# Kernel optimization log

Hardware: AMD Instinct MI355X
Metric: run time of the kernel (lower is better)

The kernel has to match this reference:

```python
import jax, jax.numpy as jnp
import numpy as np

NUM_HEADS = 32
NUM_KV_HEADS = 8
NUM_GROUPS = NUM_HEADS // NUM_KV_HEADS  # 4
HEAD_DIM = 64
HIDDEN = 2048
ROPE_THETA = 10000.0


def rotate_half(x):
    half = x.shape[-1] // 2
    x1, x2 = x[..., :half], x[..., half:]
    return jnp.concatenate([-x2, x1], axis=-1)


def rope_cos_sin(seq_len, dtype):
    inv_freq = 1.0 / (ROPE_THETA ** (jnp.arange(0, HEAD_DIM, 2, dtype=jnp.float32) / HEAD_DIM))
    pos = jnp.arange(seq_len, dtype=jnp.float32)
    freqs = jnp.outer(pos, inv_freq)          # [S, HEAD_DIM/2]
    emb = jnp.concatenate([freqs, freqs], axis=-1)  # [S, HEAD_DIM]
    return jnp.cos(emb).astype(dtype), jnp.sin(emb).astype(dtype)


def setup_inputs() -> dict:
    key = jax.random.key(0)
    k0, k1, k2, k3, k4 = jax.random.split(key, 5)
    B, S = 2, 2048
    scale = 0.02
    return {
        "hidden_states": jax.random.normal(k0, (B, S, HIDDEN), dtype=jnp.float32),
        "Wq": jax.random.normal(k1, (NUM_HEADS * HEAD_DIM, HIDDEN), dtype=jnp.float32) * scale,
        "Wk": jax.random.normal(k2, (NUM_KV_HEADS * HEAD_DIM, HIDDEN), dtype=jnp.float32) * scale,
        "Wv": jax.random.normal(k3, (NUM_KV_HEADS * HEAD_DIM, HIDDEN), dtype=jnp.float32) * scale,
        "Wo": jax.random.normal(k4, (HIDDEN, NUM_HEADS * HEAD_DIM), dtype=jnp.float32) * scale,
    }


def reference(hidden_states, Wq, Wk, Wv, Wo):
    B, S, _ = hidden_states.shape
    # projections (nn.Linear: x @ W.T)
    q = (hidden_states @ Wq.T).reshape(B, S, NUM_HEADS, HEAD_DIM).transpose(0, 2, 1, 3)
    k = (hidden_states @ Wk.T).reshape(B, S, NUM_KV_HEADS, HEAD_DIM).transpose(0, 2, 1, 3)
    v = (hidden_states @ Wv.T).reshape(B, S, NUM_KV_HEADS, HEAD_DIM).transpose(0, 2, 1, 3)

    cos, sin = rope_cos_sin(S, q.dtype)  # [S, HEAD_DIM]
    cos = cos[None, None]                # [1,1,S,HEAD_DIM]
    sin = sin[None, None]
    q = q * cos + rotate_half(q) * sin
    k = k * cos + rotate_half(k) * sin

    # GQA: repeat kv heads to match query heads (repeat_interleave on head dim)
    k = jnp.repeat(k, NUM_GROUPS, axis=1)  # [B, NUM_HEADS, S, HEAD_DIM]
    v = jnp.repeat(v, NUM_GROUPS, axis=1)

    scale = 1.0 / jnp.sqrt(jnp.asarray(HEAD_DIM, dtype=q.dtype))
    scores = jnp.einsum('bhqd,bhkd->bhqk', q, k) * scale  # [B,H,S,S]
    causal = jnp.tril(jnp.ones((S, S), dtype=bool))
    scores = jnp.where(causal[None, None], scores, jnp.asarray(-jnp.inf, dtype=scores.dtype))
    attn = jax.nn.softmax(scores, axis=-1)
    out = jnp.einsum('bhqk,bhkd->bhqd', attn, v)           # [B,H,S,D]
    out = out.transpose(0, 2, 1, 3).reshape(B, S, NUM_HEADS * HEAD_DIM)
    return out @ Wo.T
```

## Files before the change

kernel.cpp:

```cpp
#include <hip/hip_runtime.h>

#define S_LEN 2048
#define BATCH 2
#define NH 32
#define NKV 8
#define HD 64
#define HID 2048
#define NTOK (BATCH * S_LEN)
#define NQKV 3072
#define SC_Q 0.18033688011112042f

typedef __attribute__((ext_vector_type(8))) __bf16 bf16x8;
typedef __attribute__((ext_vector_type(4))) float f32x4;
typedef __attribute__((ext_vector_type(4))) float f32x4v;
typedef __attribute__((ext_vector_type(4))) ushort u16x4;

__device__ inline ushort f2b(float f) {
    union { float f; unsigned u; } x{f};
    unsigned r = (x.u + 0x7fff + ((x.u >> 16) & 1)) >> 16;
    return (ushort)r;
}
__device__ inline float b2f(ushort u) {
    union { unsigned u; float f; } x{(unsigned)u << 16};
    return x.f;
}
__device__ inline float ex2(float x) { return __builtin_amdgcn_exp2f(x); }

__global__ __launch_bounds__(256) void cvt_all(const float* __restrict__ hidden,
                                               const float* __restrict__ Wq,
                                               const float* __restrict__ Wk,
                                               const float* __restrict__ Wv,
                                               const float* __restrict__ Wo,
                                               ushort* __restrict__ hb,
                                               ushort* __restrict__ wqkv,
                                               ushort* __restrict__ wo) {
    for (int bid = blockIdx.x; bid < 18432; bid += gridDim.x) {
        const float* src;
        ushort* dst;
        int off;
        if (bid < 8192)        { src = hidden; dst = hb;                              off = bid; }
        else if (bid < 12288)  { src = Wq;     dst = wqkv;                            off = bid - 8192; }
        else if (bid < 13312)  { src = Wk;     dst = wqkv + (size_t)2048 * 2048;      off = bid - 12288; }
        else if (bid < 14336)  { src = Wv;     dst = wqkv + (size_t)2560 * 2048;      off = bid - 13312; }
        else                   { src = Wo;     dst = wo;                              off = bid - 14336; }
        size_t i = (size_t)off * 256 + threadIdx.x;
        f32x4v v = __builtin_nontemporal_load((const f32x4v*)src + i);
        u16x4 o = {f2b(v[0]), f2b(v[1]), f2b(v[2]), f2b(v[3])};
        *((u16x4*)dst + i) = o;
    }
}

__device__ inline void gl_lds16(const void* g, void* l) {
    __builtin_amdgcn_global_load_lds((const __attribute__((address_space(1))) void*)g,
                                     (__attribute__((address_space(3))) void*)l, 16, 0, 0);
}

__global__ __launch_bounds__(512, 2) void gemmQKV(const ushort* __restrict__ A,
                                                  const ushort* __restrict__ B,
                                                  ushort* __restrict__ Qd,
                                                  ushort* __restrict__ Kd,
                                                  ushort* __restrict__ Vd,
                                                  int M, int N, int K) {
    constexpr int CF = 3;
    constexpr int ABYTES = 256 * 64 * 2;
    constexpr int BBYTES = 192 * 64 * 2;
    __shared__ __align__(16) char lds[2][ABYTES + BBYTES];
    const int tid = threadIdx.x, lane = tid & 63, w = tid >> 6;
    const int wm = w >> 2, wn = w & 3, l15 = lane & 15, lg = lane >> 4;

    const int nbx = gridDim.x;
    int lid = blockIdx.y * nbx + blockIdx.x;
    const int cpx = (nbx * gridDim.y) >> 3;
    int swzb = (lid & 7) * cpx + (lid >> 3);
    const int m0 = (swzb / nbx) * 256, n0 = (swzb % nbx) * (CF * 64);

    const int srow = tid >> 3;
    const int scol = ((tid & 7) ^ (srow & 7)) * 8;
    const ushort* Ag = A + (size_t)(m0 + srow) * K + scol;
    const ushort* Bg = B + (size_t)(n0 + srow) * K + scol;

    auto stage = [&](int buf, int k0) {
        char* base = &lds[buf][0];
#pragma unroll
        for (int j = 0; j < CF; j++)
            gl_lds16(Bg + (size_t)(j * 64) * K + k0, base + ABYTES + (j * 64 + w * 8) * 128);
#pragma unroll
        for (int j = 0; j < 4; j++)
            gl_lds16(Ag + (size_t)(j * 64) * K + k0, base + (j * 64 + w * 8) * 128);
    };

    f32x4 acc[8][CF] = {};

    stage(0, 0);

    const int NT = K >> 6;
    const int sw = (l15 & 7) * 16;
    const int po0 = (lg * 16) ^ sw, po1 = (64 + lg * 16) ^ sw;

    for (int t = 0; t < NT; ++t) {
        asm volatile("s_waitcnt vmcnt(0)" ::: "memory");
        __builtin_amdgcn_s_barrier();
        __builtin_amdgcn_sched_barrier(0);
        if (t + 1 < NT) stage((t + 1) & 1, (t + 1) << 6);
        __builtin_amdgcn_sched_barrier(0);

        const char* pa = &lds[t & 1][0] + (wm * 128 + l15) * 128;
        const char* pb = &lds[t & 1][ABYTES] + (wn * CF * 16 + l15) * 128;

        bf16x8 bf_[2][CF];
#pragma unroll
        for (int j = 0; j < CF; j++) {
            bf_[0][j] = *(const bf16x8*)(pb + j * 2048 + po0);
            bf_[1][j] = *(const bf16x8*)(pb + j * 2048 + po1);
        }
        bf16x8 a_[2][8];
#pragma unroll
        for (int i = 0; i < 8; i++) {
            a_[0][i] = *(const bf16x8*)(pa + i * 2048 + po0);
            a_[1][i] = *(const bf16x8*)(pa + i * 2048 + po1);
        }
        __builtin_amdgcn_s_setprio(1);
#pragma unroll
        for (int ks = 0; ks < 2; ks++)
#pragma unroll
            for (int i = 0; i < 8; i++)
#pragma unroll
                for (int j = 0; j < CF; j++)
                    acc[i][j] = __builtin_amdgcn_mfma_f32_16x16x32_bf16(a_[ks][i], bf_[ks][j], acc[i][j], 0, 0, 0);
        __builtin_amdgcn_s_setprio(0);
    }

    const int mr = m0 + wm * 128 + lg * 4;
#pragma unroll
    for (int j = 0; j < CF; j++) {
        int cb = n0 + wn * CF * 16 + j * 16;
        ushort* dst;
        int dstride, colb;
        if (cb < 2048)      { dst = Qd; dstride = 2048; colb = cb + l15; }
        else if (cb < 2560) { dst = Kd; dstride = 512;  colb = cb - 2048 + l15; }
        else                { dst = Vd; dstride = 512;  colb = cb - 2560 + l15; }
#pragma unroll
        for (int i = 0; i < 8; i++)
#pragma unroll
            for (int r = 0; r < 4; r++)
                dst[(size_t)(mr + i * 16 + r) * dstride + colb] = f2b(acc[i][j][r]);
    }
}

__global__ __launch_bounds__(512, 2) void gemmO(const ushort* __restrict__ A,
                                                const ushort* __restrict__ B,
                                                float* __restrict__ C,
                                                int M, int N, int K) {
    constexpr int ABYTES = 128 * 64 * 2;
    constexpr int BBYTES = 256 * 64 * 2;
    __shared__ __align__(16) char lds[3][ABYTES + BBYTES];
    const int tid = threadIdx.x, lane = tid & 63, w = tid >> 6;
    const int wm = w >> 2, wn = w & 3, l15 = lane & 15, lg = lane >> 4;

    const int nbx = gridDim.x;
    int lid = blockIdx.y * nbx + blockIdx.x;
    const int cpx = (nbx * gridDim.y) >> 3;
    int swzb = (lid & 7) * cpx + (lid >> 3);
    const int m0 = (swzb / nbx) * 128, n0 = (swzb % nbx) * 256;

    const int srow = tid >> 3;
    const int scol = ((tid & 7) ^ (srow & 7)) * 8;
    const ushort* Ag = A + (size_t)(m0 + srow) * K + scol;
    const ushort* Bg = B + (size_t)(n0 + srow) * K + scol;

    auto stage = [&](int buf, int k0) {
        char* base = &lds[buf][0];
        gl_lds16(Ag + k0,                   base + (w * 8) * 128);
        gl_lds16(Ag + (size_t)64 * K + k0,  base + (64 + w * 8) * 128);
#pragma unroll
        for (int j = 0; j < 4; j++)
            gl_lds16(Bg + (size_t)(j * 64) * K + k0, base + ABYTES + (j * 64 + w * 8) * 128);
    };

    f32x4 acc[4][4] = {};

    stage(0, 0);
    stage(1, 64);

    const int NT = K >> 6;
    const int sw = (l15 & 7) * 16;
    const int po0 = (lg * 16) ^ sw, po1 = (64 + lg * 16) ^ sw;

    int i0 = 0, i1 = 1, i2 = 2;
    for (int t = 0; t < NT; ++t) {
        if (t < NT - 1) asm volatile("s_waitcnt vmcnt(6)" ::: "memory");
        else            asm volatile("s_waitcnt vmcnt(0)" ::: "memory");
        __builtin_amdgcn_s_barrier();
        __builtin_amdgcn_sched_barrier(0);
        if (t + 2 < NT) stage(i2, (t + 2) << 6);
        __builtin_amdgcn_sched_barrier(0);

        const char* pa = &lds[i0][0] + (wm * 64 + l15) * 128;
        const char* pb = &lds[i0][ABYTES] + (wn * 64 + l15) * 128;

        bf16x8 a_[2][4], b_[2][4];
#pragma unroll
        for (int i = 0; i < 4; i++) {
            a_[0][i] = *(const bf16x8*)(pa + i * 2048 + po0);
            a_[1][i] = *(const bf16x8*)(pa + i * 2048 + po1);
            b_[0][i] = *(const bf16x8*)(pb + i * 2048 + po0);
            b_[1][i] = *(const bf16x8*)(pb + i * 2048 + po1);
        }
        __builtin_amdgcn_s_setprio(1);
#pragma unroll
        for (int ks = 0; ks < 2; ks++)
#pragma unroll
            for (int i = 0; i < 4; i++)
#pragma unroll
                for (int j = 0; j < 4; j++)
                    acc[i][j] = __builtin_amdgcn_mfma_f32_16x16x32_bf16(a_[ks][i], b_[ks][j], acc[i][j], 0, 0, 0);
        __builtin_amdgcn_s_setprio(0);

        int tt = i0; i0 = i1; i1 = i2; i2 = tt;
    }

    const int mr = m0 + wm * 64 + lg * 4, nc = n0 + wn * 64 + l15;
#pragma unroll
    for (int i = 0; i < 4; i++)
#pragma unroll
        for (int j = 0; j < 4; j++)
#pragma unroll
            for (int r = 0; r < 4; r++)
                C[(size_t)(mr + i * 16 + r) * N + nc + j * 16] = acc[i][j][r];
}

__global__ __launch_bounds__(256) void rope_k(ushort* __restrict__ Kb) {
    int idx = blockIdx.x * 256 + threadIdx.x;
    int t = idx >> 5, rem = idx & 31;
    int hh = rem >> 2, q8 = rem & 3;
    float pos = (float)(t & (S_LEN - 1));
    ushort* base = Kb + (size_t)t * 512 + hh * 64 + q8 * 8;
    ushort4 v0 = *(ushort4*)base, v1 = *(ushort4*)(base + 4);
    ushort4 u0 = *(ushort4*)(base + 32), u1 = *(ushort4*)(base + 36);
    ushort lo[8] = {v0.x, v0.y, v0.z, v0.w, v1.x, v1.y, v1.z, v1.w};
    ushort hi[8] = {u0.x, u0.y, u0.z, u0.w, u1.x, u1.y, u1.z, u1.w};
#pragma unroll
    for (int e = 0; e < 8; e++) {
        float f = ex2(-(float)(q8 * 8 + e) * 0.4152410118609203f);
        float sv, cv;
        __sincosf(pos * f, &sv, &cv);
        float x1 = b2f(lo[e]), x2 = b2f(hi[e]);
        lo[e] = f2b(x1 * cv - x2 * sv);
        hi[e] = f2b(x2 * cv + x1 * sv);
    }
    *(ushort4*)base        = make_ushort4(lo[0], lo[1], lo[2], lo[3]);
    *(ushort4*)(base + 4)  = make_ushort4(lo[4], lo[5], lo[6], lo[7]);
    *(ushort4*)(base + 32) = make_ushort4(hi[0], hi[1], hi[2], hi[3]);
    *(ushort4*)(base + 36) = make_ushort4(hi[4], hi[5], hi[6], hi[7]);
}

__global__ __launch_bounds__(256) void transpose_v(const ushort* __restrict__ V,
                                                   ushort* __restrict__ Vt) {
    __shared__ ushort tile[32][33];
    int bz = blockIdx.z, b = bz >> 3, kvh = bz & 7;
    int s0 = blockIdx.x * 32, d0 = blockIdx.y * 32;
    int tx = threadIdx.x & 31, ty = threadIdx.x >> 5;
#pragma unroll
    for (int i = 0; i < 4; i++)
        tile[ty + i * 8][tx] = V[(size_t)(b * S_LEN + s0 + ty + i * 8) * 512 + kvh * 64 + d0 + tx];
    __syncthreads();
#pragma unroll
    for (int i = 0; i < 4; i++)
        Vt[((size_t)((b * 8 + kvh) * 64 + d0 + ty + i * 8)) * S_LEN + s0 + tx] = tile[tx][ty + i * 8];
}

__global__ __launch_bounds__(256) void attn_k(const ushort* __restrict__ Q,
                                              const ushort* __restrict__ Kc,
                                              const ushort* __restrict__ Vt,
                                              ushort* __restrict__ O) {
    __shared__ __align__(16) ushort K_lds[3][4096];
    __shared__ __align__(16) ushort V_lds[3][4096];
    const int lane = threadIdx.x & 63, w = threadIdx.x >> 6;
    const int l15 = lane & 15, lg = lane >> 4;

    int lid = blockIdx.y * 8 + blockIdx.x;
    int swz = (lid & 7) * 64 + (lid >> 3);
    const int ps = swz & 7;
    const int bh = swz >> 3;
    const int b = bh >> 5, h = bh & 31, kvh = h >> 2;

    const ushort* kSrc[2];
    const ushort* vSrc[2];
    int dstU[2];
#pragma unroll
    for (int j = 0; j < 2; j++) {
        int u = w * 2 + j;
        int row = u * 8 + (lane >> 3);
        int po = (lane & 7) * 16;
        int fr = ((row & 3) | (((row >> 3) & 1) << 2)) << 4;
        int dus = (po ^ fr) >> 1;
        kSrc[j] = Kc + (size_t)(b * S_LEN + row) * 512 + kvh * 64 + dus;
        vSrc[j] = Vt + ((size_t)((b * 8 + kvh) * 64 + row)) * S_LEN + dus;
        dstU[j] = u * 512;
    }

    int fr_k = ((l15 & 3) | (((l15 >> 2) & 1) << 2)) << 4;
    int kbase = 1024 * (l15 >> 2) + 128 * (l15 & 3) + ((lg * 16) ^ (fr_k & 48));
    int k6 = (fr_k >> 6) & 1;
    int kb0 = kbase + 64 * k6, kb1 = kbase + 64 * (1 - k6);
    int fr_v = ((l15 & 3) | (((l15 >> 3) & 1) << 2)) << 4;
    int vbase = 128 * l15 + ((lg * 16) ^ (fr_v & 48));
    int v6 = (fr_v >> 6) & 1;
    int vb0 = vbase + 64 * v6, vb1 = vbase + 64 * (1 - v6);

    bf16x8 onesf;
#pragma unroll
    for (int i = 0; i < 8; i++) onesf[i] = (__bf16)1.0f;

    auto ropeq = [&](bf16x8& q0, bf16x8& q1, int qrow) {
        float pos = (float)qrow;
#pragma unroll
        for (int e = 0; e < 8; e++) {
            float f = ex2(-(float)(lg * 8 + e) * 0.4152410118609203f);
            float sv, cv;
            __sincosf(pos * f, &sv, &cv);
            float x1 = (float)q0[e], x2 = (float)q1[e];
            q0[e] = (__bf16)((x1 * cv - x2 * sv) * SC_Q);
            q1[e] = (__bf16)((x2 * cv + x1 * sv) * SC_Q);
        }
    };

    for (int half = 0; half < 2; ++half) {
        const int pp = half ? (15 - ps) : ps;
        const int q0A = pp * 128 + w * 16, q0B = q0A + 64;
        const int qrowA = q0A + l15, qrowB = q0B + l15;
        const int ktA = 2 * pp, ktB = 2 * pp + 1;

        const ushort* qpA = Q + (size_t)(b * S_LEN + qrowA) * HID + h * 64 + lg * 8;
        const ushort* qpB = Q + (size_t)(b * S_LEN + qrowB) * HID + h * 64 + lg * 8;
        bf16x8 qfA0 = *(const bf16x8*)qpA, qfA1 = *(const bf16x8*)(qpA + 32);
        bf16x8 qfB0 = *(const bf16x8*)qpB, qfB1 = *(const bf16x8*)(qpB + 32);
        ropeq(qfA0, qfA1, qrowA);
        ropeq(qfB0, qfB1, qrowB);
        asm volatile("s_waitcnt vmcnt(0)" ::: "memory");

        f32x4 aoA[4] = {}, aoB[4] = {};
        f32x4 lsumA = {}, lsumB = {};

        int i0 = 0, i1 = 1, i2 = 2;
#pragma unroll
        for (int j = 0; j < 2; j++) {
            gl_lds16(kSrc[j], &K_lds[0][dstU[j]]);
            gl_lds16(vSrc[j], &V_lds[0][dstU[j]]);
        }
#pragma unroll
        for (int j = 0; j < 2; j++) {
            gl_lds16(kSrc[j] + (size_t)64 * 512, &K_lds[1][dstU[j]]);
            gl_lds16(vSrc[j] + 64, &V_lds[1][dstU[j]]);
        }

        for (int kt = 0; kt <= ktB; ++kt) {
            const int kn = kt << 6;
            if (kt < ktB) asm volatile("s_waitcnt vmcnt(4)" ::: "memory");
            else          asm volatile("s_waitcnt vmcnt(0)" ::: "memory");
            __builtin_amdgcn_s_barrier();

            if (kt + 2 <= ktB) {
                const int kn2 = kn + 128;
#pragma unroll
                for (int j = 0; j < 2; j++) {
                    gl_lds16(kSrc[j] + (size_t)kn2 * 512, &K_lds[i2][dstU[j]]);
                    gl_lds16(vSrc[j] + kn2, &V_lds[i2][dstU[j]]);
                }
            }

            const char* Kt = (const char*)&K_lds[i0][0];
            const char* Vl = (const char*)&V_lds[i0][0];
            const bool aAct = (kt <= ktA);

            bf16x8 kf0[4], kf1[4];
#pragma unroll
            for (int kc = 0; kc < 4; kc++) {
                const int kcst = 4096 * (kc >> 1) + 512 * (kc & 1);
                kf0[kc] = *(const bf16x8*)(Kt + kb0 + kcst);
                kf1[kc] = *(const bf16x8*)(Kt + kb1 + kcst);
            }

            f32x4 sB[4], sA[4];
#pragma unroll
            for (int kc = 0; kc < 4; kc++) {
                f32x4 z = {};
                z = __builtin_amdgcn_mfma_f32_16x16x32_bf16(kf0[kc], qfB0, z, 0, 0, 0);
                z = __builtin_amdgcn_mfma_f32_16x16x32_bf16(kf1[kc], qfB1, z, 0, 0, 0);
                sB[kc] = z;
            }
            if (aAct) {
#pragma unroll
                for (int kc = 0; kc < 4; kc++) {
                    f32x4 z = {};
                    z = __builtin_amdgcn_mfma_f32_16x16x32_bf16(kf0[kc], qfA0, z, 0, 0, 0);
                    z = __builtin_amdgcn_mfma_f32_16x16x32_bf16(kf1[kc], qfA1, z, 0, 0, 0);
                    sA[kc] = z;
                }
            }

            if (kt == ktB) {
#pragma unroll
                for (int kc = 0; kc < 4; kc++)
#pragma unroll
                    for (int r = 0; r < 4; r++) {
                        int kv = kn + ((kc >> 1) << 5) + (lg << 3) + ((kc & 1) << 2) + r;
                        sB[kc][r] = (kv <= qrowB) ? sB[kc][r] : -INFINITY;
                    }
            }
            if (kt == ktA) {
#pragma unroll
                for (int kc = 0; kc < 4; kc++)
#pragma unroll
                    for (int r = 0; r < 4; r++) {
                        int kv = kn + ((kc >> 1) << 5) + (lg << 3) + ((kc & 1) << 2) + r;
                        sA[kc][r] = (kv <= qrowA) ? sA[kc][r] : -INFINITY;
                    }
            }

            bf16x8 pB0, pB1, pA0, pA1;
#pragma unroll
            for (int r = 0; r < 4; r++) {
                pB0[r]     = (__bf16)ex2(sB[0][r]);
                pB0[4 + r] = (__bf16)ex2(sB[1][r]);
                pB1[r]     = (__bf16)ex2(sB[2][r]);
                pB1[4 + r] = (__bf16)ex2(sB[3][r]);
            }
            if (aAct) {
#pragma unroll
                for (int r = 0; r < 4; r++) {
                    pA0[r]     = (__bf16)ex2(sA[0][r]);
                    pA0[4 + r] = (__bf16)ex2(sA[1][r]);
                    pA1[r]     = (__bf16)ex2(sA[2][r]);
                    pA1[4 + r] = (__bf16)ex2(sA[3][r]);
                }
            }

            lsumB = __builtin_amdgcn_mfma_f32_16x16x32_bf16(pB0, onesf, lsumB, 0, 0, 0);
            lsumB = __builtin_amdgcn_mfma_f32_16x16x32_bf16(pB1, onesf, lsumB, 0, 0, 0);
            if (aAct) {
                lsumA = __builtin_amdgcn_mfma_f32_16x16x32_bf16(pA0, onesf, lsumA, 0, 0, 0);
                lsumA = __builtin_amdgcn_mfma_f32_16x16x32_bf16(pA1, onesf, lsumA, 0, 0, 0);
            }

#pragma unroll
            for (int dt = 0; dt < 4; dt++) {
                bf16x8 vf0 = *(const bf16x8*)(Vl + vb0 + dt * 2048);
                bf16x8 vf1 = *(const bf16x8*)(Vl + vb1 + dt * 2048);
                aoB[dt] = __builtin_amdgcn_mfma_f32_16x16x32_bf16(pB0, vf0, aoB[dt], 0, 0, 0);
                aoB[dt] = __builtin_amdgcn_mfma_f32_16x16x32_bf16(pB1, vf1, aoB[dt], 0, 0, 0);
                if (aAct) {
                    aoA[dt] = __builtin_amdgcn_mfma_f32_16x16x32_bf16(pA0, vf0, aoA[dt], 0, 0, 0);
                    aoA[dt] = __builtin_amdgcn_mfma_f32_16x16x32_bf16(pA1, vf1, aoA[dt], 0, 0, 0);
                }
            }

            int t = i0; i0 = i1; i1 = i2; i2 = t;
        }

        float invA[4], invB[4];
#pragma unroll
        for (int r = 0; r < 4; r++) { invA[r] = 1.0f / lsumA[r]; invB[r] = 1.0f / lsumB[r]; }
        ushort* obA = O + (size_t)(b * S_LEN + q0A + lg * 4) * HID + h * 64 + l15;
        ushort* obB = O + (size_t)(b * S_LEN + q0B + lg * 4) * HID + h * 64 + l15;
#pragma unroll
        for (int dt = 0; dt < 4; dt++)
#pragma unroll
            for (int r = 0; r < 4; r++) {
                union { __bf16 h; ushort u; } cA{(__bf16)(aoA[dt][r] * invA[r])};
                union { __bf16 h; ushort u; } cB{(__bf16)(aoB[dt][r] * invB[r])};
                obA[(size_t)r * HID + dt * 16] = cA.u;
                obB[(size_t)r * HID + dt * 16] = cB.u;
            }

        __builtin_amdgcn_s_barrier();
    }
}

extern "C" void kernel_launch(void* const* d_in, const int* in_sizes, int n_in,
                              void* d_out, int out_size, void* d_ws, size_t ws_size,
                              hipStream_t stream) {
    const float* hidden = (const float*)d_in[0];
    const float* Wq = (const float*)d_in[1];
    const float* Wk = (const float*)d_in[2];
    const float* Wv = (const float*)d_in[3];
    const float* Wo = (const float*)d_in[4];

    char* ws = (char*)d_ws;
    size_t off = 0;
    auto alloc = [&](size_t bytes) -> void* {
        void* p = ws + off;
        off += (bytes + 255) & ~(size_t)255;
        return p;
    };
    ushort* hb   = (ushort*)alloc((size_t)NTOK * HID * 2);
    ushort* wqkv = (ushort*)alloc((size_t)NQKV * 2048 * 2);
    ushort* wo   = (ushort*)alloc((size_t)2048 * 2048 * 2);
    ushort* Qb   = (ushort*)alloc((size_t)NTOK * 2048 * 2);
    ushort* Kb   = (ushort*)alloc((size_t)NTOK * 512 * 2);
    ushort* Vb   = (ushort*)alloc((size_t)NTOK * 512 * 2);
    ushort* Vtb  = (ushort*)alloc((size_t)NTOK * 512 * 2);
    ushort* AO   = (ushort*)alloc((size_t)NTOK * 2048 * 2);

    cvt_all<<<2304, 256, 0, stream>>>(hidden, Wq, Wk, Wv, Wo, hb, wqkv, wo);

    gemmQKV<<<dim3(16, 16), 512, 0, stream>>>(hb, wqkv, Qb, Kb, Vb, NTOK, NQKV, 2048);

    rope_k<<<(NTOK * 32) / 256, 256, 0, stream>>>(Kb);

    transpose_v<<<dim3(S_LEN / 32, 2, BATCH * NKV), 256, 0, stream>>>(Vb, Vtb);

    attn_k<<<dim3(8, BATCH * NH), 256, 0, stream>>>(Qb, Kb, Vtb, AO);

    gemmO<<<dim3(8, 32), 512, 0, stream>>>(AO, wo, (float*)d_out, NTOK, 2048, 2048);
}
```

Before: 160.8 us.

## Stage KV in 128-row double-buffered tiles to halve barrier count

Replaces the triple-buffered 64-row K/V pipeline with a double-buffered scheme that loads 128 KV rows per stage and runs two 64-row subphases per barrier. The causal mask is now computed from tile-local offsets, and the last tile is specialised so the A rows skip the upper half. This halves the number of waitcnt/barrier synchronisations per query block. In exchange it waits on vmcnt(0) each iteration, which reduces prefetch depth and may expose more load latency.

```diff
diff --git a/kernel.cpp b/kernel.cpp
--- a/kernel.cpp
+++ b/kernel.cpp
@@ -273,8 +273,8 @@
                                               const ushort* __restrict__ Kc,
                                               const ushort* __restrict__ Vt,
                                               ushort* __restrict__ O) {
-    __shared__ __align__(16) ushort K_lds[3][4096];
-    __shared__ __align__(16) ushort V_lds[3][4096];
+    __shared__ __align__(16) ushort K_lds[2][2][4096];
+    __shared__ __align__(16) ushort V_lds[2][2][4096];
     const int lane = threadIdx.x & 63, w = threadIdx.x >> 6;
     const int l15 = lane & 15, lg = lane >> 4;
 
@@ -325,11 +325,13 @@
         }
     };
 
+    const int mloc = w * 16 + l15;
+
     for (int half = 0; half < 2; ++half) {
         const int pp = half ? (15 - ps) : ps;
         const int q0A = pp * 128 + w * 16, q0B = q0A + 64;
         const int qrowA = q0A + l15, qrowB = q0B + l15;
-        const int ktA = 2 * pp, ktB = 2 * pp + 1;
+        const int TL = pp + 1;
 
         const ushort* qpA = Q + (size_t)(b * S_LEN + qrowA) * HID + h * 64 + lg * 8;
         const ushort* qpB = Q + (size_t)(b * S_LEN + qrowB) * HID + h * 64 + lg * 8;
@@ -342,37 +344,21 @@
         f32x4 aoA[4] = {}, aoB[4] = {};
         f32x4 lsumA = {}, lsumB = {};
 
-        int i0 = 0, i1 = 1, i2 = 2;
-#pragma unroll
-        for (int j = 0; j < 2; j++) {
-            gl_lds16(kSrc[j], &K_lds[0][dstU[j]]);
-            gl_lds16(vSrc[j], &V_lds[0][dstU[j]]);
-        }
-#pragma unroll
-        for (int j = 0; j < 2; j++) {
-            gl_lds16(kSrc[j] + (size_t)64 * 512, &K_lds[1][dstU[j]]);
-            gl_lds16(vSrc[j] + 64, &V_lds[1][dstU[j]]);
-        }
-
-        for (int kt = 0; kt <= ktB; ++kt) {
-            const int kn = kt << 6;
-            if (kt < ktB) asm volatile("s_waitcnt vmcnt(4)" ::: "memory");
-            else          asm volatile("s_waitcnt vmcnt(0)" ::: "memory");
-            __builtin_amdgcn_s_barrier();
-
-            if (kt + 2 <= ktB) {
-                const int kn2 = kn + 128;
+        auto stage128 = [&](int buf, int tIdx) {
+#pragma unroll
+            for (int hh = 0; hh < 2; hh++) {
+                const int kv0 = tIdx * 128 + hh * 64;
 #pragma unroll
                 for (int j = 0; j < 2; j++) {
-                    gl_lds16(kSrc[j] + (size_t)kn2 * 512, &K_lds[i2][dstU[j]]);
-                    gl_lds16(vSrc[j] + kn2, &V_lds[i2][dstU[j]]);
+                    gl_lds16(kSrc[j] + (size_t)kv0 * 512, &K_lds[buf][hh][dstU[j]]);
+                    gl_lds16(vSrc[j] + kv0, &V_lds[buf][hh][dstU[j]]);
                 }
             }
-
-            const char* Kt = (const char*)&K_lds[i0][0];
-            const char* Vl = (const char*)&V_lds[i0][0];
-            const bool aAct = (kt <= ktA);
-
+        };
+
+        stage128(0, 0);
+
+        auto subphase = [&](const char* Kt, const char* Vl, bool doA, bool mA, bool mB) {
             bf16x8 kf0[4], kf1[4];
 #pragma unroll
             for (int kc = 0; kc < 4; kc++) {
@@ -380,7 +366,6 @@
                 kf0[kc] = *(const bf16x8*)(Kt + kb0 + kcst);
                 kf1[kc] = *(const bf16x8*)(Kt + kb1 + kcst);
             }
-
             f32x4 sB[4], sA[4];
 #pragma unroll
             for (int kc = 0; kc < 4; kc++) {
@@ -389,7 +374,7 @@
                 z = __builtin_amdgcn_mfma_f32_16x16x32_bf16(kf1[kc], qfB1, z, 0, 0, 0);
                 sB[kc] = z;
             }
-            if (aAct) {
+            if (doA) {
 #pragma unroll
                 for (int kc = 0; kc < 4; kc++) {
                     f32x4 z = {};
@@ -398,26 +383,24 @@
                     sA[kc] = z;
                 }
             }
-
-            if (kt == ktB) {
+            if (mB) {
 #pragma unroll
                 for (int kc = 0; kc < 4; kc++)
 #pragma unroll
                     for (int r = 0; r < 4; r++) {
-                        int kv = kn + ((kc >> 1) << 5) + (lg << 3) + ((kc & 1) << 2) + r;
-                        sB[kc][r] = (kv <= qrowB) ? sB[kc][r] : -INFINITY;
+                        int kvp = ((kc >> 1) << 5) + (lg << 3) + ((kc & 1) << 2) + r;
+                        sB[kc][r] = (kvp <= mloc) ? sB[kc][r] : -INFINITY;
                     }
             }
-            if (kt == ktA) {
+            if (doA && mA) {
 #pragma unroll
                 for (int kc = 0; kc < 4; kc++)
 #pragma unroll
                     for (int r = 0; r < 4; r++) {
-                        int kv = kn + ((kc >> 1) << 5) + (lg << 3) + ((kc & 1) << 2) + r;
-                        sA[kc][r] = (kv <= qrowA) ? sA[kc][r] : -INFINITY;
+                        int kvp = ((kc >> 1) << 5) + (lg << 3) + ((kc & 1) << 2) + r;
+                        sA[kc][r] = (kvp <= mloc) ? sA[kc][r] : -INFINITY;
                     }
             }
-
             bf16x8 pB0, pB1, pA0, pA1;
 #pragma unroll
             for (int r = 0; r < 4; r++) {
@@ -426,7 +409,7 @@
                 pB1[r]     = (__bf16)ex2(sB[2][r]);
                 pB1[4 + r] = (__bf16)ex2(sB[3][r]);
             }
-            if (aAct) {
+            if (doA) {
 #pragma unroll
                 for (int r = 0; r < 4; r++) {
                     pA0[r]     = (__bf16)ex2(sA[0][r]);
@@ -435,27 +418,39 @@
                     pA1[4 + r] = (__bf16)ex2(sA[3][r]);
                 }
             }
-
             lsumB = __builtin_amdgcn_mfma_f32_16x16x32_bf16(pB0, onesf, lsumB, 0, 0, 0);
             lsumB = __builtin_amdgcn_mfma_f32_16x16x32_bf16(pB1, onesf, lsumB, 0, 0, 0);
-            if (aAct) {
+            if (doA) {
                 lsumA = __builtin_amdgcn_mfma_f32_16x16x32_bf16(pA0, onesf, lsumA, 0, 0, 0);
                 lsumA = __builtin_amdgcn_mfma_f32_16x16x32_bf16(pA1, onesf, lsumA, 0, 0, 0);
             }
-
 #pragma unroll
             for (int dt = 0; dt < 4; dt++) {
                 bf16x8 vf0 = *(const bf16x8*)(Vl + vb0 + dt * 2048);
                 bf16x8 vf1 = *(const bf16x8*)(Vl + vb1 + dt * 2048);
                 aoB[dt] = __builtin_amdgcn_mfma_f32_16x16x32_bf16(pB0, vf0, aoB[dt], 0, 0, 0);
                 aoB[dt] = __builtin_amdgcn_mfma_f32_16x16x32_bf16(pB1, vf1, aoB[dt], 0, 0, 0);
-                if (aAct) {
+                if (doA) {
                     aoA[dt] = __builtin_amdgcn_mfma_f32_16x16x32_bf16(pA0, vf0, aoA[dt], 0, 0, 0);
                     aoA[dt] = __builtin_amdgcn_mfma_f32_16x16x32_bf16(pA1, vf1, aoA[dt], 0, 0, 0);
                 }
             }
-
-            int t = i0; i0 = i1; i1 = i2; i2 = t;
+        };
+
+        for (int t = 0; t < TL; ++t) {
+            asm volatile("s_waitcnt vmcnt(0)" ::: "memory");
+            __builtin_amdgcn_s_barrier();
+            if (t + 1 < TL) stage128((t + 1) & 1, t + 1);
+
+            const bool lastT = (t == TL - 1);
+            const char* Kt0 = (const char*)&K_lds[t & 1][0][0];
+            const char* Vl0 = (const char*)&V_lds[t & 1][0][0];
+            const char* Kt1 = (const char*)&K_lds[t & 1][1][0];
+            const char* Vl1 = (const char*)&V_lds[t & 1][1][0];
+
+            subphase(Kt0, Vl0, true, lastT, false);
+            if (!lastT) subphase(Kt1, Vl1, true, false, false);
+            else        subphase(Kt1, Vl1, false, false, true);
         }
 
         float invA[4], invB[4];
```

New measurement: 161.1 us. About the same (+0.2%).
